# Kernel optimization log

Hardware: AMD Instinct MI355X
Metric: run time of the kernel (lower is better)

Reference implementation:

```python
import jax, jax.numpy as jnp
import numpy as np

N_NODES = 400000
D_IN = 256
HIDDEN = 256
BATCH = 1024


def setup_inputs() -> dict:
    key = jax.random.key(0)
    k1, k2, k3, k4 = jax.random.split(key, 4)
    x = jax.random.normal(k1, (N_NODES, D_IN), dtype=jnp.float32)
    graph_idx = jnp.sort(jax.random.randint(k2, (N_NODES,), 0, BATCH)).astype(jnp.int64)
    # Linear(-1, hidden) params
    W = jax.random.normal(k3, (HIDDEN, D_IN), dtype=jnp.float32) / np.sqrt(D_IN)
    b = jnp.zeros((HIDDEN,), dtype=jnp.float32)
    # SoftmaxAggregation learnable per-channel temperature, PyG init = 1.0
    t = jnp.ones((1, HIDDEN), dtype=jnp.float32)
    return {"x": x, "graph_idx": graph_idx, "batch_size": BATCH, "W": W, "b": b, "t": t}


def _segment_softmax(a, idx, num_segments):
    # per-segment, per-channel numerically-stable softmax (PyG softmax)
    m = jax.ops.segment_max(a, idx, num_segments=num_segments)  # [B, C]
    e = jnp.exp(a - m[idx])
    s = jax.ops.segment_sum(e, idx, num_segments=num_segments)  # [B, C]
    return e / (s[idx] + 1e-16)


def reference(x, graph_idx, batch_size, W, b, t):
    idx = graph_idx.astype(jnp.int32)
    h = jax.nn.relu(x @ W.T + b)                      # [N, C]
    alpha = _segment_softmax(h * t, idx, batch_size)  # [N, C]
    agg = jax.ops.segment_sum(h * alpha, idx, num_segments=batch_size)  # [B, C]
    # graph_tran = MLP(n_graph_trans=0, ...) is identity
    return agg.reshape(batch_size, -1)
```

## Files before the change

### kernel.cpp

```cpp
#include <hip/hip_runtime.h>
#include <hip/hip_bf16.h>


typedef __attribute__((ext_vector_type(8))) short short8;
typedef __attribute__((ext_vector_type(4))) float f32x4;
typedef __attribute__((ext_vector_type(4))) unsigned u32x4;

#define D_INN 256
#define HID 256
#define BM 32
#define NGRID 256
#define NTHREADS 512

__device__ __forceinline__ unsigned pk2(float a, float b) {
    unsigned r;
    asm("v_cvt_pk_bf16_f32 %0, %1, %2" : "=v"(r) : "v"(a), "v"(b));
    return r;
}

__global__ void conv_w(const float* __restrict__ W, short* __restrict__ Wb) {
    int i = (blockIdx.x * blockDim.x + threadIdx.x) * 8;
    float4 a = ((const float4*)(W + i))[0];
    float4 b = ((const float4*)(W + i))[1];
    uint4 o;
    o.x = pk2(a.x, a.y); o.y = pk2(a.z, a.w);
    o.z = pk2(b.x, b.y); o.w = pk2(b.z, b.w);
    *(uint4*)(Wb + i) = o;
}

__global__ void tile_meta(const int* __restrict__ gidx, uint4* __restrict__ meta) {
    const int tile = blockIdx.x;
    const int l = threadIdx.x;
    const int sid = gidx[tile * BM + (l & 31)];
    const int s0 = __shfl(sid, 0);
    const int s31 = __shfl(sid, 31);
    const unsigned long long m = __ballot(sid != s0);
    if (l == 0)
        meta[tile] = make_uint4((unsigned)s0, (unsigned)s31, (unsigned)m, 0u);
}

__global__ void zero_sp(float* __restrict__ sp) {
    int i = blockIdx.x * blockDim.x + threadIdx.x;
    ((f32x4*)sp)[i] = (f32x4){0.f, 0.f, 0.f, 0.f};
}

__global__ void finalize(const float* __restrict__ S, const float* __restrict__ P,
                         float* __restrict__ out) {
    int i = blockIdx.x * blockDim.x + threadIdx.x;
    out[i] = P[i] / (S[i] + 1e-16f);
}

__device__ __forceinline__ void issue_dma(const float* __restrict__ xtile,
                                          float* ldsbuf, int w, int l) {
#pragma unroll
    for (int i = 0; i < 4; ++i) {
        const int row = w * 4 + i;
        const int xr = (row & 7) << 4;
        const char* src = (const char*)xtile + row * 1024 + ((l * 16) ^ xr);
        __builtin_amdgcn_global_load_lds(
            (const __attribute__((address_space(1))) unsigned*)src,
            (__attribute__((address_space(3))) unsigned*)(ldsbuf + (row << 8)),
            16, 0, 0);
    }
}

template<int MODE>
__global__ __launch_bounds__(NTHREADS, 1) void gemm_fused(
    const float* __restrict__ x, const uint4* __restrict__ meta,
    const short* __restrict__ Wb, const float* __restrict__ bias,
    const float* __restrict__ temp, float* __restrict__ part, float* __restrict__ P,
    int NT)
{
    __shared__ __align__(16) float Alds[4][BM * D_INN];
    __shared__ uint4 Mlds[64];

    const int t = threadIdx.x;
    const int w = t >> 6;
    const int l = t & 63;
    const int lrow = l & 15;
    const int lq = l >> 4;

    if (t < 64) {
        const int mt_tile = blockIdx.x + t * NGRID;
        if (mt_tile < NT) Mlds[t] = meta[mt_tile];
    }

    short8 bvAll[2][8];
#pragma unroll
    for (int ni = 0; ni < 2; ++ni)
#pragma unroll
        for (int ks = 0; ks < 8; ++ks)
            bvAll[ni][ks] = *(const short8*)(Wb + (w * 32 + ni * 16 + lrow) * D_INN + ks * 32 + lq * 8);

    float bb[2], tt[2];
#pragma unroll
    for (int ni = 0; ni < 2; ++ni) {
        bb[ni] = bias[w * 32 + ni * 16 + lrow];
        tt[ni] = temp[w * 32 + ni * 16 + lrow];
    }
    const int rb0 = lrow * 1024 + ((lq * 32) ^ ((lrow & 7) << 4));

    __syncthreads();

    const int blk = blockIdx.x;
#pragma unroll
    for (int k = 0; k < 3; ++k) {
        const int tk = blk + k * NGRID;
        if (tk < NT) issue_dma(x + (long)tk * (BM * D_INN), &Alds[k][0], w, l);
    }

    for (int it = 0;; ++it) {
        const int jt = blk + it * NGRID;
        if (jt >= NT) break;
        const int pf = jt + 3 * NGRID;
        if (pf < NT)
            issue_dma(x + (long)pf * (BM * D_INN), &Alds[(it + 3) & 3][0], w, l);

        const int f = (jt + NGRID < NT) + (jt + 2 * NGRID < NT) + (jt + 3 * NGRID < NT);
        if (f == 3)      asm volatile("s_waitcnt vmcnt(12)" ::: "memory");
        else if (f == 2) asm volatile("s_waitcnt vmcnt(8)" ::: "memory");
        else if (f == 1) asm volatile("s_waitcnt vmcnt(4)" ::: "memory");
        else             asm volatile("s_waitcnt vmcnt(0)" ::: "memory");
        __builtin_amdgcn_s_barrier();
        __builtin_amdgcn_sched_barrier(0);

        const uint4 mt = Mlds[it];

        f32x4 acc[2][2];
#pragma unroll
        for (int i = 0; i < 2; ++i)
#pragma unroll
            for (int j = 0; j < 2; ++j)
                acc[i][j] = (f32x4){0.f, 0.f, 0.f, 0.f};

        const char* ldsb = (const char*)&Alds[it & 3][0];
#pragma unroll
        for (int ks = 0; ks < 8; ++ks) {
            short8 av[2];
#pragma unroll
            for (int mi = 0; mi < 2; ++mi) {
                float4 lo = *(const float4*)(ldsb + mi * 16384 + ks * 128 + rb0);
                float4 hi = *(const float4*)(ldsb + mi * 16384 + ks * 128 + (rb0 ^ 16));
                u32x4 ua;
                ua.x = pk2(lo.x, lo.y); ua.y = pk2(lo.z, lo.w);
                ua.z = pk2(hi.x, hi.y); ua.w = pk2(hi.z, hi.w);
                av[mi] = __builtin_bit_cast(short8, ua);
            }
#pragma unroll
            for (int mi = 0; mi < 2; ++mi)
#pragma unroll
                for (int ni = 0; ni < 2; ++ni)
                    acc[mi][ni] = __builtin_amdgcn_mfma_f32_16x16x32_bf16(av[mi], bvAll[ni][ks], acc[mi][ni], 0, 0, 0);
        }

        const int s0 = (int)mt.x, s31 = (int)mt.y;
        float* pb = part + ((size_t)jt << 10);

        if (mt.z == 0) {
#pragma unroll
            for (int ni = 0; ni < 2; ++ni) {
                float es = 0.f, ps = 0.f;
#pragma unroll
                for (int mi = 0; mi < 2; ++mi)
#pragma unroll
                    for (int j = 0; j < 4; ++j) {
                        float h = fmaxf(acc[mi][ni][j] + bb[ni], 0.f);
                        float e = __expf(h * tt[ni]);
                        es += e; ps += h * e;
                    }
                es += __shfl_xor(es, 16); ps += __shfl_xor(ps, 16);
                es += __shfl_xor(es, 32); ps += __shfl_xor(ps, 32);
                if (l < 16) {
                    const int ch = w * 32 + ni * 16 + lrow;
                    if (MODE == 1) {
                        atomicAdd(&part[(size_t)s0 * HID + ch], es);
                        atomicAdd(&P[(size_t)s0 * HID + ch], ps);
                    } else {
                        pb[ch] = es;
                        pb[256 + ch] = ps;
                    }
                }
            }
        } else {
            int himask = 0;
#pragma unroll
            for (int mi = 0; mi < 2; ++mi)
#pragma unroll
                for (int j = 0; j < 4; ++j)
                    if ((mt.z >> (mi * 16 + lq * 4 + j)) & 1) himask |= 1 << (mi * 4 + j);
#pragma unroll
            for (int ni = 0; ni < 2; ++ni) {
                float es0 = 0.f, ps0 = 0.f, es1 = 0.f, ps1 = 0.f;
#pragma unroll
                for (int mi = 0; mi < 2; ++mi)
#pragma unroll
                    for (int j = 0; j < 4; ++j) {
                        float h = fmaxf(acc[mi][ni][j] + bb[ni], 0.f);
                        float e = __expf(h * tt[ni]);
                        if ((himask >> (mi * 4 + j)) & 1) { es1 += e; ps1 += h * e; }
                        else                              { es0 += e; ps0 += h * e; }
                    }
                es0 += __shfl_xor(es0, 16); ps0 += __shfl_xor(ps0, 16);
                es0 += __shfl_xor(es0, 32); ps0 += __shfl_xor(ps0, 32);
                es1 += __shfl_xor(es1, 16); ps1 += __shfl_xor(ps1, 16);
                es1 += __shfl_xor(es1, 32); ps1 += __shfl_xor(ps1, 32);
                if (l < 16) {
                    const int ch = w * 32 + ni * 16 + lrow;
                    if (MODE == 1) {
                        atomicAdd(&part[(size_t)s0 * HID + ch], es0);
                        atomicAdd(&P[(size_t)s0 * HID + ch], ps0);
                        atomicAdd(&part[(size_t)s31 * HID + ch], es1);
                        atomicAdd(&P[(size_t)s31 * HID + ch], ps1);
                    } else {
                        pb[ch] = es0;
                        pb[256 + ch] = ps0;
                        pb[512 + ch] = es1;
                        pb[768 + ch] = ps1;
                    }
                }
            }
        }

        __builtin_amdgcn_s_barrier();
    }
}

__global__ void reduce_seg(const int* __restrict__ gidx, const float* __restrict__ part,
                           float* __restrict__ out, int N) {
    const int g = blockIdx.x;
    const int ch = threadIdx.x;
    int lo = 0, hi = N;
    while (lo < hi) { int m = (lo + hi) >> 1; if (gidx[m] < g) lo = m + 1; else hi = m; }
    const int r0 = lo;
    hi = N;
    while (lo < hi) { int m = (lo + hi) >> 1; if (gidx[m] < g + 1) lo = m + 1; else hi = m; }
    const int r1 = lo;
    float es = 0.f, ps = 0.f;
    if (r0 < r1) {
        const int b0 = r0 >> 5, b1 = (r1 - 1) >> 5;
        for (int b = b0; b <= b1; ++b) {
            const float* pb = part + ((size_t)b << 10);
            const int off = (gidx[b << 5] == g) ? 0 : 512;
            es += pb[off + ch];
            ps += pb[off + 256 + ch];
        }
    }
    out[(size_t)g * HID + ch] = ps / (es + 1e-16f);
}

extern "C" void kernel_launch(void* const* d_in, const int* in_sizes, int n_in,
                              void* d_out, int out_size, void* d_ws, size_t ws_size,
                              hipStream_t stream) {
    const float* x    = (const float*)d_in[0];
    const int*   gidx = (const int*)d_in[1];
    const float* W    = (const float*)d_in[3];
    const float* bias = (const float*)d_in[4];
    const float* temp = (const float*)d_in[5];
    float* out = (float*)d_out;

    const int N = in_sizes[1];
    const int B = out_size / HID;
    const int NT = N / BM;

    const size_t partFloats = (size_t)NT * 1024;
    const size_t need = partFloats * 4 + (size_t)HID * D_INN * 2 + (size_t)NT * 16;

    if (ws_size >= need) {
        float* part = (float*)d_ws;
        short* Wb = (short*)(part + partFloats);
        uint4* meta = (uint4*)(Wb + (size_t)HID * D_INN);
        conv_w<<<(HID * D_INN) / (8 * 256), 256, 0, stream>>>(W, Wb);
        tile_meta<<<NT, 64, 0, stream>>>(gidx, meta);
        gemm_fused<0><<<NGRID, NTHREADS, 0, stream>>>(x, meta, Wb, bias, temp, part, nullptr, NT);
        reduce_seg<<<B, 256, 0, stream>>>(gidx, part, out, N);
    } else {
        float* S = (float*)d_ws;
        float* P = S + (size_t)B * HID;
        short* Wb = (short*)(P + (size_t)B * HID);
        uint4* meta = (uint4*)(Wb + (size_t)HID * D_INN);
        zero_sp<<<(2 * B * HID) / (256 * 4), 256, 0, stream>>>(S);
        conv_w<<<(HID * D_INN) / (8 * 256), 256, 0, stream>>>(W, Wb);
        tile_meta<<<NT, 64, 0, stream>>>(gidx, meta);
        gemm_fused<1><<<NGRID, NTHREADS, 0, stream>>>(x, meta, Wb, bias, temp, S, P, NT);
        finalize<<<(B * HID) / 256, 256, 0, stream>>>(S, P, out);
    }
}
```

Measured before the change: 143.0 us.

## Fold weight conversion into GEMM, restructure DMA wait/barrier, interleave partial stores

Drops the separate W-to-bf16 conversion kernel and converts the fp32 weights to bf16 inside the fused GEMM prologue, saving one launch. The main loop now waits for the current tile and barriers before issuing the next prefetch, which removes the trailing per-iteration barrier. The vmcnt counts now also cover outstanding partial-result stores. Partial (exp-sum, weighted-sum) pairs are stored interleaved as float2, and the uniform-segment fast path is merged into the two-segment path. This trades a few extra ALU ops per tile for fewer barriers, fewer launches and wider stores and loads in the reduction.

Result: slower. 160.0 us (+11.9%).

```diff
diff --git a/kernel.cpp b/kernel.cpp
--- a/kernel.cpp
+++ b/kernel.cpp
@@ -3,6 +3,7 @@
 
 
 typedef __attribute__((ext_vector_type(8))) short short8;
+typedef __attribute__((ext_vector_type(2))) float f32x2;
 typedef __attribute__((ext_vector_type(4))) float f32x4;
 typedef __attribute__((ext_vector_type(4))) unsigned u32x4;
 
@@ -16,16 +17,6 @@
     unsigned r;
     asm("v_cvt_pk_bf16_f32 %0, %1, %2" : "=v"(r) : "v"(a), "v"(b));
     return r;
-}
-
-__global__ void conv_w(const float* __restrict__ W, short* __restrict__ Wb) {
-    int i = (blockIdx.x * blockDim.x + threadIdx.x) * 8;
-    float4 a = ((const float4*)(W + i))[0];
-    float4 b = ((const float4*)(W + i))[1];
-    uint4 o;
-    o.x = pk2(a.x, a.y); o.y = pk2(a.z, a.w);
-    o.z = pk2(b.x, b.y); o.w = pk2(b.z, b.w);
-    *(uint4*)(Wb + i) = o;
 }
 
 __global__ void tile_meta(const int* __restrict__ gidx, uint4* __restrict__ meta) {
@@ -67,7 +58,7 @@
 template<int MODE>
 __global__ __launch_bounds__(NTHREADS, 1) void gemm_fused(
     const float* __restrict__ x, const uint4* __restrict__ meta,
-    const short* __restrict__ Wb, const float* __restrict__ bias,
+    const float* __restrict__ W, const float* __restrict__ bias,
     const float* __restrict__ temp, float* __restrict__ part, float* __restrict__ P,
     int NT)
 {
@@ -79,9 +70,10 @@
     const int l = t & 63;
     const int lrow = l & 15;
     const int lq = l >> 4;
+    const int blk = blockIdx.x;
 
     if (t < 64) {
-        const int mt_tile = blockIdx.x + t * NGRID;
+        const int mt_tile = blk + t * NGRID;
         if (mt_tile < NT) Mlds[t] = meta[mt_tile];
     }
 
@@ -89,8 +81,15 @@
 #pragma unroll
     for (int ni = 0; ni < 2; ++ni)
 #pragma unroll
-        for (int ks = 0; ks < 8; ++ks)
-            bvAll[ni][ks] = *(const short8*)(Wb + (w * 32 + ni * 16 + lrow) * D_INN + ks * 32 + lq * 8);
+        for (int ks = 0; ks < 8; ++ks) {
+            const float* wp = W + (size_t)(w * 32 + ni * 16 + lrow) * D_INN + ks * 32 + lq * 8;
+            float4 a = ((const float4*)wp)[0];
+            float4 b = ((const float4*)wp)[1];
+            u32x4 ua;
+            ua.x = pk2(a.x, a.y); ua.y = pk2(a.z, a.w);
+            ua.z = pk2(b.x, b.y); ua.w = pk2(b.z, b.w);
+            bvAll[ni][ks] = __builtin_bit_cast(short8, ua);
+        }
 
     float bb[2], tt[2];
 #pragma unroll
@@ -102,7 +101,6 @@
 
     __syncthreads();
 
-    const int blk = blockIdx.x;
 #pragma unroll
     for (int k = 0; k < 3; ++k) {
         const int tk = blk + k * NGRID;
@@ -112,16 +110,28 @@
     for (int it = 0;; ++it) {
         const int jt = blk + it * NGRID;
         if (jt >= NT) break;
+
+        if (MODE == 1) {
+            asm volatile("s_waitcnt vmcnt(0)" ::: "memory");
+        } else {
+            const int b2 = (jt + NGRID < NT) + (jt + 2 * NGRID < NT);
+            const int sg = it < 3 ? it : 3;
+            const int n = b2 * 4 + sg * 4;
+            switch (n) {
+                case 20: asm volatile("s_waitcnt vmcnt(20)" ::: "memory"); break;
+                case 16: asm volatile("s_waitcnt vmcnt(16)" ::: "memory"); break;
+                case 12: asm volatile("s_waitcnt vmcnt(12)" ::: "memory"); break;
+                case 8:  asm volatile("s_waitcnt vmcnt(8)"  ::: "memory"); break;
+                case 4:  asm volatile("s_waitcnt vmcnt(4)"  ::: "memory"); break;
+                default: asm volatile("s_waitcnt vmcnt(0)"  ::: "memory"); break;
+            }
+        }
+        __builtin_amdgcn_s_barrier();
+        __builtin_amdgcn_sched_barrier(0);
+
         const int pf = jt + 3 * NGRID;
         if (pf < NT)
             issue_dma(x + (long)pf * (BM * D_INN), &Alds[(it + 3) & 3][0], w, l);
-
-        const int f = (jt + NGRID < NT) + (jt + 2 * NGRID < NT) + (jt + 3 * NGRID < NT);
-        if (f == 3)      asm volatile("s_waitcnt vmcnt(12)" ::: "memory");
-        else if (f == 2) asm volatile("s_waitcnt vmcnt(8)" ::: "memory");
-        else if (f == 1) asm volatile("s_waitcnt vmcnt(4)" ::: "memory");
-        else             asm volatile("s_waitcnt vmcnt(0)" ::: "memory");
-        __builtin_amdgcn_s_barrier();
         __builtin_amdgcn_sched_barrier(0);
 
         const uint4 mt = Mlds[it];
@@ -156,72 +166,44 @@
         const int s0 = (int)mt.x, s31 = (int)mt.y;
         float* pb = part + ((size_t)jt << 10);
 
-        if (mt.z == 0) {
-#pragma unroll
-            for (int ni = 0; ni < 2; ++ni) {
-                float es = 0.f, ps = 0.f;
-#pragma unroll
-                for (int mi = 0; mi < 2; ++mi)
-#pragma unroll
-                    for (int j = 0; j < 4; ++j) {
-                        float h = fmaxf(acc[mi][ni][j] + bb[ni], 0.f);
-                        float e = __expf(h * tt[ni]);
-                        es += e; ps += h * e;
-                    }
-                es += __shfl_xor(es, 16); ps += __shfl_xor(ps, 16);
-                es += __shfl_xor(es, 32); ps += __shfl_xor(ps, 32);
-                if (l < 16) {
-                    const int ch = w * 32 + ni * 16 + lrow;
-                    if (MODE == 1) {
-                        atomicAdd(&part[(size_t)s0 * HID + ch], es);
-                        atomicAdd(&P[(size_t)s0 * HID + ch], ps);
-                    } else {
-                        pb[ch] = es;
-                        pb[256 + ch] = ps;
-                    }
+        int himask = 0;
+#pragma unroll
+        for (int mi = 0; mi < 2; ++mi)
+#pragma unroll
+            for (int j = 0; j < 4; ++j)
+                if ((mt.z >> (mi * 16 + lq * 4 + j)) & 1) himask |= 1 << (mi * 4 + j);
+
+#pragma unroll
+        for (int ni = 0; ni < 2; ++ni) {
+            float es0 = 0.f, ps0 = 0.f, es1 = 0.f, ps1 = 0.f;
+#pragma unroll
+            for (int mi = 0; mi < 2; ++mi)
+#pragma unroll
+                for (int j = 0; j < 4; ++j) {
+                    float h = fmaxf(acc[mi][ni][j] + bb[ni], 0.f);
+                    float e = __expf(h * tt[ni]);
+                    if ((himask >> (mi * 4 + j)) & 1) { es1 += e; ps1 += h * e; }
+                    else                              { es0 += e; ps0 += h * e; }
+                }
+            es0 += __shfl_xor(es0, 16); ps0 += __shfl_xor(ps0, 16);
+            es0 += __shfl_xor(es0, 32); ps0 += __shfl_xor(ps0, 32);
+            es1 += __shfl_xor(es1, 16); ps1 += __shfl_xor(ps1, 16);
+            es1 += __shfl_xor(es1, 32); ps1 += __shfl_xor(ps1, 32);
+            if (l < 16) {
+                const int ch = w * 32 + ni * 16 + lrow;
+                if (MODE == 1) {
+                    atomicAdd(&part[(size_t)s0 * HID + ch], es0);
+                    atomicAdd(&P[(size_t)s0 * HID + ch], ps0);
+                    atomicAdd(&part[(size_t)s31 * HID + ch], es1);
+                    atomicAdd(&P[(size_t)s31 * HID + ch], ps1);
+                } else {
+                    f32x2 v0; v0.x = es0; v0.y = ps0;
+                    f32x2 v1; v1.x = es1; v1.y = ps1;
+                    *(f32x2*)&pb[2 * ch] = v0;
+                    *(f32x2*)&pb[512 + 2 * ch] = v1;
                 }
             }
-        } else {
-            int himask = 0;
-#pragma unroll
-            for (int mi = 0; mi < 2; ++mi)
-#pragma unroll
-                for (int j = 0; j < 4; ++j)
-                    if ((mt.z >> (mi * 16 + lq * 4 + j)) & 1) himask |= 1 << (mi * 4 + j);
-#pragma unroll
-            for (int ni = 0; ni < 2; ++ni) {
-                float es0 = 0.f, ps0 = 0.f, es1 = 0.f, ps1 = 0.f;
-#pragma unroll
-                for (int mi = 0; mi < 2; ++mi)
-#pragma unroll
-                    for (int j = 0; j < 4; ++j) {
-                        float h = fmaxf(acc[mi][ni][j] + bb[ni], 0.f);
-                        float e = __expf(h * tt[ni]);
-                        if ((himask >> (mi * 4 + j)) & 1) { es1 += e; ps1 += h * e; }
-                        else                              { es0 += e; ps0 += h * e; }
-                    }
-                es0 += __shfl_xor(es0, 16); ps0 += __shfl_xor(ps0, 16);
-                es0 += __shfl_xor(es0, 32); ps0 += __shfl_xor(ps0, 32);
-                es1 += __shfl_xor(es1, 16); ps1 += __shfl_xor(ps1, 16);
-                es1 += __shfl_xor(es1, 32); ps1 += __shfl_xor(ps1, 32);
-                if (l < 16) {
-                    const int ch = w * 32 + ni * 16 + lrow;
-                    if (MODE == 1) {
-                        atomicAdd(&part[(size_t)s0 * HID + ch], es0);
-                        atomicAdd(&P[(size_t)s0 * HID + ch], ps0);
-                        atomicAdd(&part[(size_t)s31 * HID + ch], es1);
-                        atomicAdd(&P[(size_t)s31 * HID + ch], ps1);
-                    } else {
-                        pb[ch] = es0;
-                        pb[256 + ch] = ps0;
-                        pb[512 + ch] = es1;
-                        pb[768 + ch] = ps1;
-                    }
-                }
-            }
-        }
-
-        __builtin_amdgcn_s_barrier();
+        }
     }
 }
 
@@ -239,10 +221,11 @@
     if (r0 < r1) {
         const int b0 = r0 >> 5, b1 = (r1 - 1) >> 5;
         for (int b = b0; b <= b1; ++b) {
-            const float* pb = part + ((size_t)b << 10);
-            const int off = (gidx[b << 5] == g) ? 0 : 512;
-            es += pb[off + ch];
-            ps += pb[off + 256 + ch];
+            const f32x2* pb = (const f32x2*)(part + ((size_t)b << 10));
+            const int off = (gidx[b << 5] == g) ? 0 : 256;
+            f32x2 v = pb[off + ch];
+            es += v.x;
+            ps += v.y;
         }
     }
     out[(size_t)g * HID + ch] = ps / (es + 1e-16f);
@@ -263,25 +246,21 @@
     const int NT = N / BM;
 
     const size_t partFloats = (size_t)NT * 1024;
-    const size_t need = partFloats * 4 + (size_t)HID * D_INN * 2 + (size_t)NT * 16;
+    const size_t need = partFloats * 4 + (size_t)NT * 16;
 
     if (ws_size >= need) {
         float* part = (float*)d_ws;
-        short* Wb = (short*)(part + partFloats);
-        uint4* meta = (uint4*)(Wb + (size_t)HID * D_INN);
-        conv_w<<<(HID * D_INN) / (8 * 256), 256, 0, stream>>>(W, Wb);
+        uint4* meta = (uint4*)(part + partFloats);
         tile_meta<<<NT, 64, 0, stream>>>(gidx, meta);
-        gemm_fused<0><<<NGRID, NTHREADS, 0, stream>>>(x, meta, Wb, bias, temp, part, nullptr, NT);
+        gemm_fused<0><<<NGRID, NTHREADS, 0, stream>>>(x, meta, W, bias, temp, part, nullptr, NT);
         reduce_seg<<<B, 256, 0, stream>>>(gidx, part, out, N);
     } else {
         float* S = (float*)d_ws;
         float* P = S + (size_t)B * HID;
-        short* Wb = (short*)(P + (size_t)B * HID);
-        uint4* meta = (uint4*)(Wb + (size_t)HID * D_INN);
+        uint4* meta = (uint4*)(P + (size_t)B * HID);
         zero_sp<<<(2 * B * HID) / (256 * 4), 256, 0, stream>>>(S);
-        conv_w<<<(HID * D_INN) / (8 * 256), 256, 0, stream>>>(W, Wb);
         tile_meta<<<NT, 64, 0, stream>>>(gidx, meta);
-        gemm_fused<1><<<NGRID, NTHREADS, 0, stream>>>(x, meta, Wb, bias, temp, S, P, NT);
+        gemm_fused<1><<<NGRID, NTHREADS, 0, stream>>>(x, meta, W, bias, temp, S, P, NT);
         finalize<<<(B * HID) / 256, 256, 0, stream>>>(S, P, out);
     }
 }
```
